# Performance work log

Measured on AMD Instinct MI355X. Metric: run time of the kernel, lower is better.

The kernel has to match this reference:

```python
import jax, jax.numpy as jnp
import numpy as np

N_NODES = 100000


def setup_inputs() -> dict:
    key = jax.random.key(0)
    k1, k2, k3, k4, k5 = jax.random.split(key, 5)
    in_f, out_f, E = 128, 128, 1600000
    std = 1.0 / np.sqrt(out_f)
    H = jax.random.normal(k1, (N_NODES, in_f), dtype=jnp.float32)
    W = jax.random.uniform(k2, (in_f, out_f), minval=-std, maxval=std, dtype=jnp.float32)
    bias = jax.random.uniform(k3, (out_f,), minval=-std, maxval=std, dtype=jnp.float32)
    row = jax.random.randint(k4, (E,), 0, N_NODES, dtype=jnp.int32)
    col = jax.random.randint(k5, (E,), 0, N_NODES, dtype=jnp.int32)
    return {"H": H, "W": W, "bias": bias, "row": row, "col": col}


def reference(H, W, bias, row, col):
    # H: [N, in_f]; W: [in_f, out_f]; row/col: [E] edge endpoints
    Hp = jnp.matmul(H, W)  # [N, out_f]
    # edge-wise attention: leaky_relu(<Hp[i], Hp[j]>)
    scores = jax.nn.leaky_relu(jnp.sum(Hp[row] * Hp[col], axis=-1), negative_slope=0.2)  # [E]
    # scatter-softmax over rows (matches sparse_softmax: exp / (row_sum + 1e-10))
    ex = jnp.exp(scores)
    denom = jax.ops.segment_sum(ex, row, num_segments=N_NODES)  # [N]
    attn = ex / (denom[row] + 1e-10)  # [E]
    # sparse-matmul aggregation: out[i] = sum_e attn[e] * Hp[col[e]]
    out = jax.ops.segment_sum(attn[:, None] * Hp[col], row, num_segments=N_NODES)  # [N, out_f]
    return out + bias
```

## Files before the change

kernel.cpp:

```cpp
#include <hip/hip_runtime.h>
#include <hip/hip_bf16.h>

#define RSH 7
#define RPB (1 << RSH)
#define CSH 17
#define CMASK ((1 << CSH) - 1)
#define CHUNK_E 8192
#define CAP 4096

__device__ __forceinline__ unsigned short f2bf(float f) {
    unsigned int u = __float_as_uint(f);
    u += 0x7FFFu + ((u >> 16) & 1u);
    return (unsigned short)(u >> 16);
}
__device__ __forceinline__ float bf2f(unsigned short h) {
    return __uint_as_float((unsigned int)h << 16);
}

typedef __attribute__((ext_vector_type(8))) short bf16x8;
typedef __attribute__((ext_vector_type(4))) float f32x4;
typedef __attribute__((ext_vector_type(2))) float f32x2;

__global__ __launch_bounds__(512) void gemm_hist(
    const float* __restrict__ H, const float* __restrict__ Wg,
    unsigned short* __restrict__ Hpb, int N,
    const int* __restrict__ row, unsigned short* __restrict__ Ht,
    int E, int nchunk, int nb2, int gemmBlocks)
{
    __shared__ unsigned short Ahi[128 * 128];
    __shared__ unsigned short Alo[128 * 128];
    __shared__ unsigned short Whi[128 * 128];
    __shared__ unsigned short Wlo[128 * 128];
    const int tid = threadIdx.x;

    if (blockIdx.x >= gemmBlocks) {
        int* cnt = (int*)Ahi;
        const int c = blockIdx.x - gemmBlocks;
        for (int i = tid; i < nb2; i += 512) cnt[i] = 0;
        __syncthreads();
        const int e0 = c * CHUNK_E;
        const int e1 = min(e0 + CHUNK_E, E);
        for (int e = e0 + tid; e < e1; e += 512)
            atomicAdd(&cnt[row[e] >> RSH], 1);
        __syncthreads();
        for (int i = tid; i < nb2; i += 512)
            Ht[(size_t)i * nchunk + c] = (unsigned short)cnt[i];
        return;
    }

    const int rbase = blockIdx.x * 128;

    #pragma unroll
    for (int i = 0; i < 4; ++i) {
        int task = tid + 512 * i;
        int n  = task & 127;
        int k0 = (task >> 7) * 8;
        unsigned int hi[4], lo[4];
        #pragma unroll
        for (int j = 0; j < 4; ++j) {
            float w0 = Wg[(size_t)(k0 + 2*j)     * 128 + n];
            float w1 = Wg[(size_t)(k0 + 2*j + 1) * 128 + n];
            unsigned short h0 = f2bf(w0), h1 = f2bf(w1);
            unsigned short l0 = f2bf(w0 - bf2f(h0)), l1 = f2bf(w1 - bf2f(h1));
            hi[j] = (unsigned int)h0 | ((unsigned int)h1 << 16);
            lo[j] = (unsigned int)l0 | ((unsigned int)l1 << 16);
        }
        int byte = (k0 * 2) ^ ((n & 7) << 4);
        *(uint4*)((char*)Whi + n * 256 + byte) = make_uint4(hi[0], hi[1], hi[2], hi[3]);
        *(uint4*)((char*)Wlo + n * 256 + byte) = make_uint4(lo[0], lo[1], lo[2], lo[3]);
    }
    #pragma unroll
    for (int i = 0; i < 8; ++i) {
        int flat = tid + 512 * i;
        int rr = flat >> 5;
        int c4  = (flat & 31) * 4;
        float4 h = make_float4(0.f, 0.f, 0.f, 0.f);
        if (rbase + rr < N)
            h = *(const float4*)&H[(size_t)(rbase + rr) * 128 + c4];
        unsigned short h0 = f2bf(h.x), h1 = f2bf(h.y), h2 = f2bf(h.z), h3 = f2bf(h.w);
        uint2 vh, vl;
        vh.x = (unsigned int)h0 | ((unsigned int)h1 << 16);
        vh.y = (unsigned int)h2 | ((unsigned int)h3 << 16);
        vl.x = (unsigned int)f2bf(h.x - bf2f(h0)) | ((unsigned int)f2bf(h.y - bf2f(h1)) << 16);
        vl.y = (unsigned int)f2bf(h.z - bf2f(h2)) | ((unsigned int)f2bf(h.w - bf2f(h3)) << 16);
        int byte = (c4 * 2) ^ ((rr & 7) << 4);
        *(uint2*)((char*)Ahi + rr * 256 + byte) = vh;
        *(uint2*)((char*)Alo + rr * 256 + byte) = vl;
    }
    __syncthreads();

    const int wid = tid >> 6, lane = tid & 63;
    const int wm = wid >> 1, wn = wid & 1;
    const int lr = lane & 15, lg = lane >> 4;
    f32x4 acc[2][4] = {};

    #pragma unroll
    for (int ks = 0; ks < 4; ++ks) {
        const int kb = ks * 64 + lg * 16;
        bf16x8 ahi[2], alo[2];
        #pragma unroll
        for (int mi = 0; mi < 2; ++mi) {
            int rr = wm * 32 + mi * 16 + lr;
            int sw = kb ^ ((rr & 7) << 4);
            ahi[mi] = *(const bf16x8*)((char*)Ahi + rr * 256 + sw);
            alo[mi] = *(const bf16x8*)((char*)Alo + rr * 256 + sw);
        }
        #pragma unroll
        for (int nf = 0; nf < 4; ++nf) {
            int n = wn * 64 + nf * 16 + lr;
            int sw = kb ^ ((n & 7) << 4);
            bf16x8 bhi = *(const bf16x8*)((char*)Whi + n * 256 + sw);
            bf16x8 blo = *(const bf16x8*)((char*)Wlo + n * 256 + sw);
            #pragma unroll
            for (int mi = 0; mi < 2; ++mi) {
                acc[mi][nf] = __builtin_amdgcn_mfma_f32_16x16x32_bf16(ahi[mi], bhi, acc[mi][nf], 0, 0, 0);
                acc[mi][nf] = __builtin_amdgcn_mfma_f32_16x16x32_bf16(ahi[mi], blo, acc[mi][nf], 0, 0, 0);
                acc[mi][nf] = __builtin_amdgcn_mfma_f32_16x16x32_bf16(alo[mi], bhi, acc[mi][nf], 0, 0, 0);
            }
        }
    }

    #pragma unroll
    for (int mi = 0; mi < 2; ++mi) {
        #pragma unroll
        for (int nf = 0; nf < 4; ++nf) {
            int col = wn * 64 + nf * 16 + lr;
            #pragma unroll
            for (int i = 0; i < 4; ++i) {
                int rr = rbase + wm * 32 + mi * 16 + lg * 4 + i;
                if (rr < N)
                    Hpb[(size_t)rr * 128 + col] = f2bf(acc[mi][nf][i]);
            }
        }
    }
}

__global__ __launch_bounds__(256) void bucket_scan(
    const unsigned short* __restrict__ Ht, unsigned short* __restrict__ rel,
    int* __restrict__ totals, int nchunk)
{
    __shared__ int s[256];
    const int b = blockIdx.x, tid = threadIdx.x;
    int v = (tid < nchunk) ? (int)Ht[(size_t)b * nchunk + tid] : 0;
    s[tid] = v;
    __syncthreads();
    for (int d = 1; d < 256; d <<= 1) {
        int t = (tid >= d) ? s[tid - d] : 0;
        __syncthreads();
        s[tid] += t;
        __syncthreads();
    }
    if (tid < nchunk) rel[(size_t)b * nchunk + tid] = (unsigned short)(s[tid] - v);
    if (tid == 255) totals[b] = s[255];
}

__global__ __launch_bounds__(1024) void bucket_ptr_scan(
    const int* __restrict__ totals, int* __restrict__ bucketptr, int nb2)
{
    __shared__ int s[1024];
    const int tid = threadIdx.x;
    int v = (tid < nb2) ? totals[tid] : 0;
    s[tid] = v;
    __syncthreads();
    for (int d = 1; d < 1024; d <<= 1) {
        int t = (tid >= d) ? s[tid - d] : 0;
        __syncthreads();
        s[tid] += t;
        __syncthreads();
    }
    if (tid < nb2) bucketptr[tid] = s[tid] - v;
    if (tid == nb2 - 1) bucketptr[nb2] = s[tid];
}

__global__ __launch_bounds__(256) void chunk_scatter(
    const int* __restrict__ row, const int* __restrict__ col,
    const unsigned short* __restrict__ rel, const int* __restrict__ bucketptr,
    int* __restrict__ colsort, int E, int nchunk, int nb2)
{
    __shared__ int loc[1025];
    __shared__ int cur[1024];
    __shared__ int gb[1024];
    __shared__ unsigned short bid[CHUNK_E];
    __shared__ int ord[CHUNK_E];
    __shared__ int part[256];
    const int tid = threadIdx.x;
    const int c = blockIdx.x;
    const int e0 = c * CHUNK_E;
    const int tot = min(CHUNK_E, E - e0);

    for (int i = tid; i < nb2; i += 256) loc[i] = 0;
    __syncthreads();
    for (int j = tid; j < tot; j += 256)
        atomicAdd(&loc[row[e0 + j] >> RSH], 1);
    __syncthreads();

    const int base = tid * 4;
    int v[4]; int s = 0;
    #pragma unroll
    for (int i = 0; i < 4; ++i) {
        int idx = base + i;
        v[i] = (idx < nb2) ? loc[idx] : 0;
        s += v[i];
    }
    part[tid] = s;
    __syncthreads();
    for (int d = 1; d < 256; d <<= 1) {
        int t = (tid >= d) ? part[tid - d] : 0;
        __syncthreads();
        part[tid] += t;
        __syncthreads();
    }
    int run = part[tid] - s;
    #pragma unroll
    for (int i = 0; i < 4; ++i) {
        int idx = base + i;
        if (idx < nb2) { loc[idx] = run; cur[idx] = run; }
        run += v[i];
    }
    if (tid == 255) loc[nb2] = part[255];
    __syncthreads();

    for (int b = tid; b < nb2; b += 256) {
        gb[b] = bucketptr[b] + (int)rel[(size_t)b * nchunk + c];
        int st = loc[b], en = loc[b + 1];
        for (int j = st; j < en; ++j) bid[j] = (unsigned short)b;
    }
    __syncthreads();

    for (int j = tid; j < tot; j += 256) {
        int r = row[e0 + j], cc = col[e0 + j];
        int b = r >> RSH;
        int p = atomicAdd(&cur[b], 1);
        ord[p] = ((r & (RPB - 1)) << CSH) | cc;
    }
    __syncthreads();

    for (int j = tid; j < tot; j += 256) {
        int b = bid[j];
        colsort[gb[b] + (j - loc[b])] = ord[j];
    }
}

__global__ __launch_bounds__(256) void bucket_sort(
    const int* __restrict__ bucketptr, int* __restrict__ rowptr,
    int* __restrict__ colsort, int N)
{
    __shared__ int rcnt[RPB];
    __shared__ int rcur[RPB];
    __shared__ int sc[256];
    __shared__ int ord[CAP];
    const int b = blockIdx.x, tid = threadIdx.x;
    const int rbase = b << RSH;
    const int s0 = bucketptr[b];
    const int cnt = bucketptr[b + 1] - s0;

    if (tid < RPB) rcnt[tid] = 0;
    __syncthreads();
    for (int j = tid; j < cnt; j += 256)
        atomicAdd(&rcnt[colsort[s0 + j] >> CSH], 1);
    __syncthreads();

    int v = (tid < RPB) ? rcnt[tid] : 0;
    sc[tid] = v;
    __syncthreads();
    for (int d = 1; d < RPB; d <<= 1) {
        int t = (tid >= d) ? sc[tid - d] : 0;
        __syncthreads();
        sc[tid] += t;
        __syncthreads();
    }
    if (tid < RPB) {
        int ex = sc[tid] - v;
        rcur[tid] = ex;
        int r = rbase + tid;
        if (r < N) rowptr[r] = s0 + ex;
    }
    if (tid == RPB - 1) {
        int rend = min(rbase + RPB, N);
        rowptr[rend] = s0 + cnt;
    }
    __syncthreads();

    for (int j = tid; j < cnt; j += 256) {
        int rec = colsort[s0 + j];
        int p = atomicAdd(&rcur[rec >> CSH], 1);
        ord[p] = rec & CMASK;
    }
    __syncthreads();
    for (int j = tid; j < cnt; j += 256)
        colsort[s0 + j] = ord[j];
}

__device__ __forceinline__ void unpack8v(uint4 v, f32x2* p) {
    p[0] = (f32x2){__uint_as_float(v.x << 16), __uint_as_float(v.x & 0xFFFF0000u)};
    p[1] = (f32x2){__uint_as_float(v.y << 16), __uint_as_float(v.y & 0xFFFF0000u)};
    p[2] = (f32x2){__uint_as_float(v.z << 16), __uint_as_float(v.z & 0xFFFF0000u)};
    p[3] = (f32x2){__uint_as_float(v.w << 16), __uint_as_float(v.w & 0xFFFF0000u)};
}

__global__ __launch_bounds__(256) void aggregate_kernel(
    const unsigned short* __restrict__ Hpb, const int* __restrict__ rowptr,
    const int* __restrict__ cols, const float* __restrict__ bias,
    float* __restrict__ out, int N)
{
    const int lane = threadIdx.x & 63;
    const int wv   = threadIdx.x >> 6;
    const int r = blockIdx.x * 4 + wv;
    if (r >= N) return;
    const int d = lane & 15;
    const int g = lane >> 4;

    const float4* bp = (const float4*)&bias[d * 8];
    const float4 b0 = bp[0], b1 = bp[1];

    f32x2 hr2[4];
    unpack8v(*(const uint4*)&Hpb[(size_t)r * 128 + d * 8], hr2);

    f32x2 acc2[4] = {};
    float den = 0.f;
    const int e0 = rowptr[r], e1 = rowptr[r + 1];
    const int elast = e1 - 1;

    for (int e = e0 + g; e < e1; e += 8) {
        const bool m1 = (e + 4 < e1);
        const int ea = e;
        const int eb = m1 ? e + 4 : elast;
        int c0 = cols[ea];
        int c1 = cols[eb];
        uint4 v0 = *(const uint4*)&Hpb[(size_t)c0 * 128 + d * 8];
        uint4 v1 = *(const uint4*)&Hpb[(size_t)c1 * 128 + d * 8];
        f32x2 hc0[4], hc1[4];
        unpack8v(v0, hc0);
        unpack8v(v1, hc1);

        f32x2 dp0 = hr2[0] * hc0[0];
        f32x2 dp1 = hr2[0] * hc1[0];
        dp0 += hr2[1] * hc0[1];
        dp1 += hr2[1] * hc1[1];
        dp0 += hr2[2] * hc0[2];
        dp1 += hr2[2] * hc1[2];
        dp0 += hr2[3] * hc0[3];
        dp1 += hr2[3] * hc1[3];
        float dot0 = dp0.x + dp0.y;
        float dot1 = dp1.x + dp1.y;

        dot0 += __shfl_xor(dot0, 1);
        dot1 += __shfl_xor(dot1, 1);
        dot0 += __shfl_xor(dot0, 2);
        dot1 += __shfl_xor(dot1, 2);
        dot0 += __shfl_xor(dot0, 4);
        dot1 += __shfl_xor(dot1, 4);
        dot0 += __shfl_xor(dot0, 8);
        dot1 += __shfl_xor(dot1, 8);

        float s0 = fmaxf(dot0, 0.2f * dot0);
        float s1 = fmaxf(dot1, 0.2f * dot1);
        float ex0 = __expf(s0);
        float ex1 = m1 ? __expf(s1) : 0.f;
        den += ex0 + ex1;
        #pragma unroll
        for (int k = 0; k < 4; ++k) {
            acc2[k] += hc0[k] * ex0;
            acc2[k] += hc1[k] * ex1;
        }
    }

    #pragma unroll
    for (int k = 0; k < 4; ++k) {
        acc2[k].x += __shfl_xor(acc2[k].x, 16);
        acc2[k].y += __shfl_xor(acc2[k].y, 16);
        acc2[k].x += __shfl_xor(acc2[k].x, 32);
        acc2[k].y += __shfl_xor(acc2[k].y, 32);
    }
    den += __shfl_xor(den, 16);
    den += __shfl_xor(den, 32);

    if (g == 0) {
        float inv = 1.f / (den + 1e-10f);
        float4 o0, o1;
        o0.x = fmaf(acc2[0].x, inv, b0.x);
        o0.y = fmaf(acc2[0].y, inv, b0.y);
        o0.z = fmaf(acc2[1].x, inv, b0.z);
        o0.w = fmaf(acc2[1].y, inv, b0.w);
        o1.x = fmaf(acc2[2].x, inv, b1.x);
        o1.y = fmaf(acc2[2].y, inv, b1.y);
        o1.z = fmaf(acc2[3].x, inv, b1.z);
        o1.w = fmaf(acc2[3].y, inv, b1.w);
        float4* op = (float4*)&out[(size_t)r * 128 + d * 8];
        op[0] = o0;
        op[1] = o1;
    }
}

extern "C" void kernel_launch(void* const* d_in, const int* in_sizes, int n_in,
                              void* d_out, int out_size, void* d_ws, size_t ws_size,
                              hipStream_t stream)
{
    const float* H    = (const float*)d_in[0];
    const float* W    = (const float*)d_in[1];
    const float* bias = (const float*)d_in[2];
    const int*   row  = (const int*)d_in[3];
    const int*   col  = (const int*)d_in[4];
    const int N = in_sizes[0] / 128;
    const int E = in_sizes[3];

    const int nchunk = (E + CHUNK_E - 1) / CHUNK_E;
    const int nb2    = (N + RPB - 1) / RPB;

    auto align = [](size_t x) { return (x + 255) & ~(size_t)255; };

    char* ws = (char*)d_ws;
    size_t off = 0;
    unsigned short* Hpb       = (unsigned short*)(ws + off); off = align(off + (size_t)N * 128 * 2);
    unsigned short* Ht        = (unsigned short*)(ws + off); off = align(off + (size_t)nb2 * nchunk * 2);
    unsigned short* rel       = (unsigned short*)(ws + off); off = align(off + (size_t)nb2 * nchunk * 2);
    int*            totals    = (int*)(ws + off);            off = align(off + (size_t)nb2 * 4);
    int*            bucketptr = (int*)(ws + off);            off = align(off + (size_t)(nb2 + 1) * 4);
    int*            rowptr    = (int*)(ws + off);            off = align(off + (size_t)(N + 1) * 4);
    int*            colsort   = (int*)(ws + off);

    const int gemmBlocks = (N + 127) / 128;

    gemm_hist<<<gemmBlocks + nchunk, 512, 0, stream>>>(H, W, Hpb, N,
                                                       row, Ht, E, nchunk, nb2,
                                                       gemmBlocks);
    bucket_scan<<<nb2, 256, 0, stream>>>(Ht, rel, totals, nchunk);
    bucket_ptr_scan<<<1, 1024, 0, stream>>>(totals, bucketptr, nb2);
    chunk_scatter<<<nchunk, 256, 0, stream>>>(row, col, rel, bucketptr,
                                              colsort, E, nchunk, nb2);
    bucket_sort<<<nb2, 256, 0, stream>>>(bucketptr, rowptr, colsort, N);
    aggregate_kernel<<<(N + 3) / 4, 256, 0, stream>>>(Hpb, rowptr, colsort, bias,
                                                      (float*)d_out, N);
}
```

Measured before the change: 142.0 us.

## Balance aggregation work by edge count with persistent waves over row ranges

Adds a binary-search partition kernel that splits the rows into contiguous ranges holding roughly equal numbers of edges, one range per wavefront. The aggregate kernel becomes persistent with a fixed grid of 2048 blocks, and each wave loops over its assigned rows. This is meant to cut block launch and scheduling overhead from 25k blocks and to even out per-wave load. It costs an extra kernel launch and serial row loops that may lose some latency hiding.

```diff
diff --git a/kernel.cpp b/kernel.cpp
--- a/kernel.cpp
+++ b/kernel.cpp
@@ -7,6 +7,7 @@
 #define CMASK ((1 << CSH) - 1)
 #define CHUNK_E 8192
 #define CAP 4096
+#define AGG_BLOCKS 2048
 
 __device__ __forceinline__ unsigned short f2bf(float f) {
     unsigned int u = __float_as_uint(f);
@@ -291,6 +292,22 @@
         colsort[s0 + j] = ord[j];
 }
 
+__global__ __launch_bounds__(256) void wave_part(
+    const int* __restrict__ rowptr, int* __restrict__ wstart,
+    int N, long long E, int nw)
+{
+    int w = blockIdx.x * 256 + threadIdx.x;
+    if (w > nw) return;
+    if (w == nw) { wstart[nw] = N; return; }
+    long long thr = (long long)w * E;
+    int lo = 0, hi = N;
+    while (lo < hi) {
+        int mid = (lo + hi) >> 1;
+        if ((long long)rowptr[mid] * nw >= thr) hi = mid; else lo = mid + 1;
+    }
+    wstart[w] = lo;
+}
+
 __device__ __forceinline__ void unpack8v(uint4 v, f32x2* p) {
     p[0] = (f32x2){__uint_as_float(v.x << 16), __uint_as_float(v.x & 0xFFFF0000u)};
     p[1] = (f32x2){__uint_as_float(v.y << 16), __uint_as_float(v.y & 0xFFFF0000u)};
@@ -301,94 +318,97 @@
 __global__ __launch_bounds__(256) void aggregate_kernel(
     const unsigned short* __restrict__ Hpb, const int* __restrict__ rowptr,
     const int* __restrict__ cols, const float* __restrict__ bias,
-    float* __restrict__ out, int N)
+    const int* __restrict__ wstart, float* __restrict__ out, int N)
 {
     const int lane = threadIdx.x & 63;
     const int wv   = threadIdx.x >> 6;
-    const int r = blockIdx.x * 4 + wv;
-    if (r >= N) return;
+    const int wid  = blockIdx.x * 4 + wv;
     const int d = lane & 15;
     const int g = lane >> 4;
 
+    const int r0 = wstart[wid];
+    const int r1 = wstart[wid + 1];
+
     const float4* bp = (const float4*)&bias[d * 8];
     const float4 b0 = bp[0], b1 = bp[1];
 
-    f32x2 hr2[4];
-    unpack8v(*(const uint4*)&Hpb[(size_t)r * 128 + d * 8], hr2);
-
-    f32x2 acc2[4] = {};
-    float den = 0.f;
-    const int e0 = rowptr[r], e1 = rowptr[r + 1];
-    const int elast = e1 - 1;
-
-    for (int e = e0 + g; e < e1; e += 8) {
-        const bool m1 = (e + 4 < e1);
-        const int ea = e;
-        const int eb = m1 ? e + 4 : elast;
-        int c0 = cols[ea];
-        int c1 = cols[eb];
-        uint4 v0 = *(const uint4*)&Hpb[(size_t)c0 * 128 + d * 8];
-        uint4 v1 = *(const uint4*)&Hpb[(size_t)c1 * 128 + d * 8];
-        f32x2 hc0[4], hc1[4];
-        unpack8v(v0, hc0);
-        unpack8v(v1, hc1);
-
-        f32x2 dp0 = hr2[0] * hc0[0];
-        f32x2 dp1 = hr2[0] * hc1[0];
-        dp0 += hr2[1] * hc0[1];
-        dp1 += hr2[1] * hc1[1];
-        dp0 += hr2[2] * hc0[2];
-        dp1 += hr2[2] * hc1[2];
-        dp0 += hr2[3] * hc0[3];
-        dp1 += hr2[3] * hc1[3];
-        float dot0 = dp0.x + dp0.y;
-        float dot1 = dp1.x + dp1.y;
-
-        dot0 += __shfl_xor(dot0, 1);
-        dot1 += __shfl_xor(dot1, 1);
-        dot0 += __shfl_xor(dot0, 2);
-        dot1 += __shfl_xor(dot1, 2);
-        dot0 += __shfl_xor(dot0, 4);
-        dot1 += __shfl_xor(dot1, 4);
-        dot0 += __shfl_xor(dot0, 8);
-        dot1 += __shfl_xor(dot1, 8);
-
-        float s0 = fmaxf(dot0, 0.2f * dot0);
-        float s1 = fmaxf(dot1, 0.2f * dot1);
-        float ex0 = __expf(s0);
-        float ex1 = m1 ? __expf(s1) : 0.f;
-        den += ex0 + ex1;
+    for (int r = r0; r < r1; ++r) {
+        f32x2 hr2[4];
+        unpack8v(*(const uint4*)&Hpb[(size_t)r * 128 + d * 8], hr2);
+
+        f32x2 acc2[4] = {};
+        float den = 0.f;
+        const int e0 = rowptr[r], e1 = rowptr[r + 1];
+        const int elast = e1 - 1;
+
+        for (int e = e0 + g; e < e1; e += 8) {
+            const bool m1 = (e + 4 < e1);
+            const int eb = m1 ? e + 4 : elast;
+            int c0 = cols[e];
+            int c1 = cols[eb];
+            uint4 v0 = *(const uint4*)&Hpb[(size_t)c0 * 128 + d * 8];
+            uint4 v1 = *(const uint4*)&Hpb[(size_t)c1 * 128 + d * 8];
+            f32x2 hc0[4], hc1[4];
+            unpack8v(v0, hc0);
+            unpack8v(v1, hc1);
+
+            f32x2 dp0 = hr2[0] * hc0[0];
+            f32x2 dp1 = hr2[0] * hc1[0];
+            dp0 += hr2[1] * hc0[1];
+            dp1 += hr2[1] * hc1[1];
+            dp0 += hr2[2] * hc0[2];
+            dp1 += hr2[2] * hc1[2];
+            dp0 += hr2[3] * hc0[3];
+            dp1 += hr2[3] * hc1[3];
+            float dot0 = dp0.x + dp0.y;
+            float dot1 = dp1.x + dp1.y;
+
+            dot0 += __shfl_xor(dot0, 1);
+            dot1 += __shfl_xor(dot1, 1);
+            dot0 += __shfl_xor(dot0, 2);
+            dot1 += __shfl_xor(dot1, 2);
+            dot0 += __shfl_xor(dot0, 4);
+            dot1 += __shfl_xor(dot1, 4);
+            dot0 += __shfl_xor(dot0, 8);
+            dot1 += __shfl_xor(dot1, 8);
+
+            float s0 = fmaxf(dot0, 0.2f * dot0);
+            float s1 = fmaxf(dot1, 0.2f * dot1);
+            float ex0 = __expf(s0);
+            float ex1 = m1 ? __expf(s1) : 0.f;
+            den += ex0 + ex1;
+            #pragma unroll
+            for (int k = 0; k < 4; ++k) {
+                acc2[k] += hc0[k] * ex0;
+                acc2[k] += hc1[k] * ex1;
+            }
+        }
+
         #pragma unroll
         for (int k = 0; k < 4; ++k) {
-            acc2[k] += hc0[k] * ex0;
-            acc2[k] += hc1[k] * ex1;
-        }
-    }
-
-    #pragma unroll
-    for (int k = 0; k < 4; ++k) {
-        acc2[k].x += __shfl_xor(acc2[k].x, 16);
-        acc2[k].y += __shfl_xor(acc2[k].y, 16);
-        acc2[k].x += __shfl_xor(acc2[k].x, 32);
-        acc2[k].y += __shfl_xor(acc2[k].y, 32);
-    }
-    den += __shfl_xor(den, 16);
-    den += __shfl_xor(den, 32);
-
-    if (g == 0) {
-        float inv = 1.f / (den + 1e-10f);
-        float4 o0, o1;
-        o0.x = fmaf(acc2[0].x, inv, b0.x);
-        o0.y = fmaf(acc2[0].y, inv, b0.y);
-        o0.z = fmaf(acc2[1].x, inv, b0.z);
-        o0.w = fmaf(acc2[1].y, inv, b0.w);
-        o1.x = fmaf(acc2[2].x, inv, b1.x);
-        o1.y = fmaf(acc2[2].y, inv, b1.y);
-        o1.z = fmaf(acc2[3].x, inv, b1.z);
-        o1.w = fmaf(acc2[3].y, inv, b1.w);
-        float4* op = (float4*)&out[(size_t)r * 128 + d * 8];
-        op[0] = o0;
-        op[1] = o1;
+            acc2[k].x += __shfl_xor(acc2[k].x, 16);
+            acc2[k].y += __shfl_xor(acc2[k].y, 16);
+            acc2[k].x += __shfl_xor(acc2[k].x, 32);
+            acc2[k].y += __shfl_xor(acc2[k].y, 32);
+        }
+        den += __shfl_xor(den, 16);
+        den += __shfl_xor(den, 32);
+
+        if (g == 0) {
+            float inv = 1.f / (den + 1e-10f);
+            float4 o0, o1;
+            o0.x = fmaf(acc2[0].x, inv, b0.x);
+            o0.y = fmaf(acc2[0].y, inv, b0.y);
+            o0.z = fmaf(acc2[1].x, inv, b0.z);
+            o0.w = fmaf(acc2[1].y, inv, b0.w);
+            o1.x = fmaf(acc2[2].x, inv, b1.x);
+            o1.y = fmaf(acc2[2].y, inv, b1.y);
+            o1.z = fmaf(acc2[3].x, inv, b1.z);
+            o1.w = fmaf(acc2[3].y, inv, b1.w);
+            float4* op = (float4*)&out[(size_t)r * 128 + d * 8];
+            op[0] = o0;
+            op[1] = o1;
+        }
     }
 }
 
@@ -406,6 +426,7 @@
 
     const int nchunk = (E + CHUNK_E - 1) / CHUNK_E;
     const int nb2    = (N + RPB - 1) / RPB;
+    const int nw     = AGG_BLOCKS * 4;
 
     auto align = [](size_t x) { return (x + 255) & ~(size_t)255; };
 
@@ -417,6 +438,7 @@
     int*            totals    = (int*)(ws + off);            off = align(off + (size_t)nb2 * 4);
     int*            bucketptr = (int*)(ws + off);            off = align(off + (size_t)(nb2 + 1) * 4);
     int*            rowptr    = (int*)(ws + off);            off = align(off + (size_t)(N + 1) * 4);
+    int*            wstart    = (int*)(ws + off);            off = align(off + (size_t)(nw + 1) * 4);
     int*            colsort   = (int*)(ws + off);
 
     const int gemmBlocks = (N + 127) / 128;
@@ -429,6 +451,8 @@
     chunk_scatter<<<nchunk, 256, 0, stream>>>(row, col, rel, bucketptr,
                                               colsort, E, nchunk, nb2);
     bucket_sort<<<nb2, 256, 0, stream>>>(bucketptr, rowptr, colsort, N);
-    aggregate_kernel<<<(N + 3) / 4, 256, 0, stream>>>(Hpb, rowptr, colsort, bias,
-                                                      (float*)d_out, N);
-}
+    wave_part<<<(nw + 256) / 256, 256, 0, stream>>>(rowptr, wstart, N,
+                                                    (long long)E, nw);
+    aggregate_kernel<<<AGG_BLOCKS, 256, 0, stream>>>(Hpb, rowptr, colsort, bias,
+                                                     wstart, (float*)d_out, N);
+}
```

New measurement: 172.9 us. +21.7%, slower.
